# Optimization experiments

Hardware: AMD Instinct MI355X
Metric: run time of the kernel (lower is better)

Reference implementation:

```python
import jax, jax.numpy as jnp
import numpy as np

CODEBOOK_SIZE = 1024
CODEWORD_SIZE = 256
BETA = 0.1
N_INIT = 1  # embedding ~ U(-1/n, 1/n)


def setup_inputs() -> dict:
    key = jax.random.key(0)
    kx, ke = jax.random.split(key)
    x = jax.random.normal(kx, (16, 4096, CODEWORD_SIZE), dtype=jnp.float32)
    embedding = jax.random.uniform(
        ke, (CODEBOOK_SIZE, CODEWORD_SIZE), dtype=jnp.float32,
        minval=-1.0 / N_INIT, maxval=1.0 / N_INIT)
    return {"x": x, "embedding": embedding}


def reference(x, embedding):
    dist = (jnp.sum(x * x, axis=2, keepdims=True)
            + jnp.sum(embedding * embedding, axis=1)
            - 2.0 * jnp.einsum('btd,kd->btk', x, embedding))
    indexes = jnp.argmin(dist, axis=2)              # [B,T] int
    values = jnp.take(embedding, indexes, axis=0)   # gather == one_hot @ embedding
    sg = jax.lax.stop_gradient
    loss1 = jnp.mean((sg(x) - values) ** 2)         # codebook loss
    loss2 = jnp.mean((x - sg(values)) ** 2)         # commitment loss
    loss = loss1 + BETA * loss2
    values_st = x + sg(values - x)                  # straight-through
    return values_st, indexes, loss
```

## Files before the change

kernel.cpp:

```cpp
#include <hip/hip_runtime.h>
#include <stdint.h>


#define BT    65536
#define D     256
#define KCB   1024
#define BM    256
#define BN    256
#define NT    (KCB/BN)
#define BK    32
#define NSTEP (NT * (D / BK))

typedef float    f32x4 __attribute__((ext_vector_type(4)));
typedef _Float16 f16x8 __attribute__((ext_vector_type(8)));

#define GLOAD_LDS16(g, l) \
  __builtin_amdgcn_global_load_lds((const __attribute__((address_space(1))) void*)(g), \
                                   (__attribute__((address_space(3))) void*)(l), 16, 0, 0)

__global__ __launch_bounds__(256) void split_kernel(const float* __restrict__ src,
                                                    _Float16* __restrict__ dh,
                                                    _Float16* __restrict__ dl,
                                                    float* __restrict__ norm) {
    const int r = blockIdx.x * 8 + (threadIdx.x >> 5);
    const size_t i0 = (size_t)r * D + (threadIdx.x & 31) * 8;
    float4 v0 = *(const float4*)(src + i0);
    float4 v1 = *(const float4*)(src + i0 + 4);
    float v[8] = {v0.x, v0.y, v0.z, v0.w, v1.x, v1.y, v1.z, v1.w};
    f16x8 h, l;
    float s = 0.f;
    #pragma unroll
    for (int j = 0; j < 8; ++j) {
        _Float16 hh = (_Float16)v[j];
        h[j] = hh;
        l[j] = (_Float16)(v[j] - (float)hh);
        s += v[j] * v[j];
    }
    *(f16x8*)(dh + i0) = h;
    *(f16x8*)(dl + i0) = l;
    #pragma unroll
    for (int off = 1; off < 32; off <<= 1) s += __shfl_xor(s, off, 64);
    if ((threadIdx.x & 31) == 0) norm[r] = s;
}

__global__ __launch_bounds__(512, 2) void vq_mfma_kernel(
    const _Float16* __restrict__ Xh, const _Float16* __restrict__ Xl,
    const _Float16* __restrict__ Eh, const _Float16* __restrict__ El,
    const float* __restrict__ enorm, const float* __restrict__ xnorm,
    const float* __restrict__ E,
    float* __restrict__ out_vals, float* __restrict__ out_idx,
    float* __restrict__ out_loss) {
    __shared__ __align__(16) _Float16 Ash[2][BM * BK];
    __shared__ __align__(16) _Float16 Asl[2][BM * BK];
    __shared__ __align__(16) _Float16 Bsh[2][BN * BK];
    __shared__ __align__(16) _Float16 Bsl[2][BN * BK];
    __shared__ float s_en[KCB];
    __shared__ float s_bd[BM];
    __shared__ int   s_bi[BM];
    __shared__ float s_red[8];

    const int tid  = threadIdx.x;
    const int w    = tid >> 6;
    const int lane = tid & 63;
    const int quad = lane >> 4;
    const int l16  = lane & 15;
    const int wm   = w >> 1;
    const int wn   = w & 1;
    const int row0 = blockIdx.x * BM;

    const int sr = lane >> 2;
    const int sk = ((((lane & 3) - (lane >> 3)) & 3) << 3);
    const int kob = ((quad + ((l16 >> 1) & 3)) & 3) << 3;

    s_en[tid]       = enorm[tid];
    s_en[tid + 512] = enorm[tid + 512];

    auto STAGE = [&](int buf, int s) {
        const int kb   = (s & 7) * BK;
        const int col0 = (s >> 3) * BN;
        #pragma unroll
        for (int t = 0; t < 2; ++t) {
            const int chunk = w * 2 + t;
            const int gr = chunk * 16 + sr;
            const size_t ga = (size_t)(row0 + gr) * D + kb + sk;
            GLOAD_LDS16(Xh + ga, &Ash[buf][chunk * 512]);
            GLOAD_LDS16(Xl + ga, &Asl[buf][chunk * 512]);
            const size_t gb = (size_t)(col0 + gr) * D + kb + sk;
            GLOAD_LDS16(Eh + gb, &Bsh[buf][chunk * 512]);
            GLOAD_LDS16(El + gb, &Bsl[buf][chunk * 512]);
        }
    };

    float rb_d[4][4];
    int   rb_i[4][4];
    #pragma unroll
    for (int i = 0; i < 4; ++i)
        #pragma unroll
        for (int r = 0; r < 4; ++r) { rb_d[i][r] = 3.4e38f; rb_i[i][r] = 0; }
    f32x4 acc[4][8];

    STAGE(0, 0);
    asm volatile("s_waitcnt lgkmcnt(0)" ::: "memory");

    #pragma unroll 2
    for (int s = 0; s < NSTEP; ++s) {
        const int cur = s & 1;
        if (s + 1 < NSTEP) {
            STAGE(cur ^ 1, s + 1);
            asm volatile("s_waitcnt vmcnt(8)" ::: "memory");
        } else {
            asm volatile("s_waitcnt vmcnt(0)" ::: "memory");
        }
        __builtin_amdgcn_s_barrier();

        if ((s & 7) == 0) {
            #pragma unroll
            for (int i = 0; i < 4; ++i)
                #pragma unroll
                for (int j = 0; j < 8; ++j) acc[i][j] = (f32x4)0.0f;
        }

        const _Float16* Ah = Ash[cur];
        const _Float16* Al = Asl[cur];
        const _Float16* Bh = Bsh[cur];
        const _Float16* Bl = Bsl[cur];

        f16x8 ah[4], al[4];
        #pragma unroll
        for (int i = 0; i < 4; ++i) {
            const int ra = (wm * 64 + i * 16 + l16) * BK + kob;
            ah[i] = *(const f16x8*)&Ah[ra];
            al[i] = *(const f16x8*)&Al[ra];
        }

        __builtin_amdgcn_s_setprio(1);
        #pragma unroll
        for (int j = 0; j < 8; ++j) {
            const int n = (wn * 128 + j * 16 + l16) * BK + kob;
            const f16x8 bh = *(const f16x8*)&Bh[n];
            const f16x8 bl = *(const f16x8*)&Bl[n];
            #pragma unroll
            for (int i = 0; i < 4; ++i) {
                acc[i][j] = __builtin_amdgcn_mfma_f32_16x16x32_f16(ah[i], bh, acc[i][j], 0, 0, 0);
                acc[i][j] = __builtin_amdgcn_mfma_f32_16x16x32_f16(al[i], bh, acc[i][j], 0, 0, 0);
                acc[i][j] = __builtin_amdgcn_mfma_f32_16x16x32_f16(ah[i], bl, acc[i][j], 0, 0, 0);
            }
        }
        __builtin_amdgcn_s_setprio(0);

        if ((s & 7) == 7) {
            const int nt = s >> 3;
            #pragma unroll
            for (int j = 0; j < 8; ++j) {
                const int c = nt * BN + wn * 128 + j * 16 + l16;
                const float en = s_en[c];
                #pragma unroll
                for (int i = 0; i < 4; ++i)
                    #pragma unroll
                    for (int r = 0; r < 4; ++r) {
                        const float sd = en - 2.0f * acc[i][j][r];
                        if (sd < rb_d[i][r]) { rb_d[i][r] = sd; rb_i[i][r] = c; }
                    }
            }
        }
        __builtin_amdgcn_s_barrier();
    }

    #pragma unroll
    for (int off = 1; off < 16; off <<= 1) {
        #pragma unroll
        for (int i = 0; i < 4; ++i)
            #pragma unroll
            for (int r = 0; r < 4; ++r) {
                const float od = __shfl_xor(rb_d[i][r], off, 64);
                const int   oi = __shfl_xor(rb_i[i][r], off, 64);
                if (od < rb_d[i][r] || (od == rb_d[i][r] && oi < rb_i[i][r])) {
                    rb_d[i][r] = od; rb_i[i][r] = oi;
                }
            }
    }
    if (wn == 0 && l16 == 0) {
        #pragma unroll
        for (int i = 0; i < 4; ++i)
            #pragma unroll
            for (int r = 0; r < 4; ++r) {
                const int m = wm * 64 + i * 16 + quad * 4 + r;
                s_bd[m] = rb_d[i][r]; s_bi[m] = rb_i[i][r];
            }
    }
    __syncthreads();
    if (wn == 1 && l16 == 0) {
        #pragma unroll
        for (int i = 0; i < 4; ++i)
            #pragma unroll
            for (int r = 0; r < 4; ++r) {
                const int m = wm * 64 + i * 16 + quad * 4 + r;
                if (rb_d[i][r] < s_bd[m] || (rb_d[i][r] == s_bd[m] && rb_i[i][r] < s_bi[m])) {
                    s_bd[m] = rb_d[i][r]; s_bi[m] = rb_i[i][r];
                }
            }
    }
    __syncthreads();

    float part = 0.f;
    if (tid < BM) {
        out_idx[row0 + tid] = (float)s_bi[tid];
        part = xnorm[row0 + tid] + s_bd[tid];
    }

    const int col = tid & 255;
    const int sub = tid >> 8;
    #pragma unroll 4
    for (int it = 0; it < BM / 2; ++it) {
        const int r  = it * 2 + sub;
        const int bi = s_bi[r];
        out_vals[(size_t)(row0 + r) * D + col] = E[(size_t)bi * D + col];
    }

    #pragma unroll
    for (int off = 1; off < 64; off <<= 1) part += __shfl_xor(part, off, 64);
    if (lane == 0) s_red[w] = part;
    __syncthreads();
    if (tid == 0) {
        float tot = 0.f;
        #pragma unroll
        for (int i = 0; i < 8; ++i) tot += s_red[i];
        atomicAdd(out_loss, tot * (1.1f / 16777216.f));
    }
}

extern "C" void kernel_launch(void* const* d_in, const int* in_sizes, int n_in,
                              void* d_out, int out_size, void* d_ws, size_t ws_size,
                              hipStream_t stream) {
    const float* X = (const float*)d_in[0];
    const float* E = (const float*)d_in[1];
    float* out      = (float*)d_out;
    float* out_vals = out;
    float* out_idx  = out + (size_t)BT * D;
    float* out_loss = out + (size_t)BT * D + BT;

    char* ws = (char*)d_ws;
    _Float16* Eh    = (_Float16*)ws;
    _Float16* El    = Eh + (size_t)KCB * D;
    _Float16* Xh    = El + (size_t)KCB * D;
    _Float16* Xl    = Xh + (size_t)BT * D;
    float*    enorm = (float*)(Xl + (size_t)BT * D);
    float*    xnorm = enorm + KCB;
    (void)ws_size; (void)n_in; (void)in_sizes; (void)out_size;

    hipMemsetAsync(out_loss, 0, sizeof(float), stream);
    split_kernel<<<KCB / 8, 256, 0, stream>>>(E, Eh, El, enorm);
    split_kernel<<<BT / 8, 256, 0, stream>>>(X, Xh, Xl, xnorm);
    vq_mfma_kernel<<<BT / BM, 512, 0, stream>>>(Xh, Xl, Eh, El, enorm, xnorm, E,
                                                out_vals, out_idx, out_loss);
}
```

Baseline: 228.8 us.

## Fuse X fp16 split into GEMM kernel and pair MFMA groups with barriers

```diff
diff --git a/kernel.cpp b/kernel.cpp
--- a/kernel.cpp
+++ b/kernel.cpp
@@ -18,14 +18,16 @@
   __builtin_amdgcn_global_load_lds((const __attribute__((address_space(1))) void*)(g), \
                                    (__attribute__((address_space(3))) void*)(l), 16, 0, 0)
 
-__global__ __launch_bounds__(256) void split_kernel(const float* __restrict__ src,
-                                                    _Float16* __restrict__ dh,
-                                                    _Float16* __restrict__ dl,
-                                                    float* __restrict__ norm) {
+__global__ __launch_bounds__(256) void split_e_kernel(const float* __restrict__ E,
+                                                      _Float16* __restrict__ Eh,
+                                                      _Float16* __restrict__ El,
+                                                      float* __restrict__ enorm,
+                                                      float* __restrict__ out_loss) {
+    if (blockIdx.x == 0 && threadIdx.x == 0) *out_loss = 0.f;
     const int r = blockIdx.x * 8 + (threadIdx.x >> 5);
     const size_t i0 = (size_t)r * D + (threadIdx.x & 31) * 8;
-    float4 v0 = *(const float4*)(src + i0);
-    float4 v1 = *(const float4*)(src + i0 + 4);
+    float4 v0 = *(const float4*)(E + i0);
+    float4 v1 = *(const float4*)(E + i0 + 4);
     float v[8] = {v0.x, v0.y, v0.z, v0.w, v1.x, v1.y, v1.z, v1.w};
     f16x8 h, l;
     float s = 0.f;
@@ -36,22 +38,20 @@
         l[j] = (_Float16)(v[j] - (float)hh);
         s += v[j] * v[j];
     }
-    *(f16x8*)(dh + i0) = h;
-    *(f16x8*)(dl + i0) = l;
+    *(f16x8*)(Eh + i0) = h;
+    *(f16x8*)(El + i0) = l;
     #pragma unroll
     for (int off = 1; off < 32; off <<= 1) s += __shfl_xor(s, off, 64);
-    if ((threadIdx.x & 31) == 0) norm[r] = s;
+    if ((threadIdx.x & 31) == 0) enorm[r] = s;
 }
 
 __global__ __launch_bounds__(512, 2) void vq_mfma_kernel(
-    const _Float16* __restrict__ Xh, const _Float16* __restrict__ Xl,
+    const float* __restrict__ X,
     const _Float16* __restrict__ Eh, const _Float16* __restrict__ El,
-    const float* __restrict__ enorm, const float* __restrict__ xnorm,
-    const float* __restrict__ E,
+    const float* __restrict__ enorm, const float* __restrict__ E,
     float* __restrict__ out_vals, float* __restrict__ out_idx,
     float* __restrict__ out_loss) {
-    __shared__ __align__(16) _Float16 Ash[2][BM * BK];
-    __shared__ __align__(16) _Float16 Asl[2][BM * BK];
+    __shared__ __align__(16) float    Asf[2][BM * BK];
     __shared__ __align__(16) _Float16 Bsh[2][BN * BK];
     __shared__ __align__(16) _Float16 Bsl[2][BN * BK];
     __shared__ float s_en[KCB];
@@ -66,10 +66,13 @@
     const int l16  = lane & 15;
     const int wm   = w >> 1;
     const int wn   = w & 1;
+    const int sxa  = l16 & 7;
     const int row0 = blockIdx.x * BM;
 
-    const int sr = lane >> 2;
-    const int sk = ((((lane & 3) - (lane >> 3)) & 3) << 3);
+    const int sa_row = lane >> 3;
+    const int sa_off = ((lane & 7) ^ sa_row) * 4;
+    const int sb_row = lane >> 2;
+    const int sb_off = ((((lane & 3) - (lane >> 3)) & 3) << 3);
     const int kob = ((quad + ((l16 >> 1) & 3)) & 3) << 3;
 
     s_en[tid]       = enorm[tid];
@@ -79,13 +82,16 @@
         const int kb   = (s & 7) * BK;
         const int col0 = (s >> 3) * BN;
         #pragma unroll
+        for (int t = 0; t < 4; ++t) {
+            const int chunk = w * 4 + t;
+            const int gr = row0 + chunk * 8 + sa_row;
+            GLOAD_LDS16(X + (size_t)gr * D + kb + sa_off, &Asf[buf][chunk * 256]);
+        }
+        #pragma unroll
         for (int t = 0; t < 2; ++t) {
             const int chunk = w * 2 + t;
-            const int gr = chunk * 16 + sr;
-            const size_t ga = (size_t)(row0 + gr) * D + kb + sk;
-            GLOAD_LDS16(Xh + ga, &Ash[buf][chunk * 512]);
-            GLOAD_LDS16(Xl + ga, &Asl[buf][chunk * 512]);
-            const size_t gb = (size_t)(col0 + gr) * D + kb + sk;
+            const int gr = col0 + chunk * 16 + sb_row;
+            const size_t gb = (size_t)gr * D + kb + sb_off;
             GLOAD_LDS16(Eh + gb, &Bsh[buf][chunk * 512]);
             GLOAD_LDS16(El + gb, &Bsl[buf][chunk * 512]);
         }
@@ -97,6 +103,7 @@
     for (int i = 0; i < 4; ++i)
         #pragma unroll
         for (int r = 0; r < 4; ++r) { rb_d[i][r] = 3.4e38f; rb_i[i][r] = 0; }
+    float xs = 0.f;
     f32x4 acc[4][8];
 
     STAGE(0, 0);
@@ -120,33 +127,55 @@
                 for (int j = 0; j < 8; ++j) acc[i][j] = (f32x4)0.0f;
         }
 
-        const _Float16* Ah = Ash[cur];
-        const _Float16* Al = Asl[cur];
+        const float*    As = Asf[cur];
         const _Float16* Bh = Bsh[cur];
         const _Float16* Bl = Bsl[cur];
 
         f16x8 ah[4], al[4];
         #pragma unroll
         for (int i = 0; i < 4; ++i) {
-            const int ra = (wm * 64 + i * 16 + l16) * BK + kob;
-            ah[i] = *(const f16x8*)&Ah[ra];
-            al[i] = *(const f16x8*)&Al[ra];
-        }
-
-        __builtin_amdgcn_s_setprio(1);
-        #pragma unroll
-        for (int j = 0; j < 8; ++j) {
-            const int n = (wn * 128 + j * 16 + l16) * BK + kob;
-            const f16x8 bh = *(const f16x8*)&Bh[n];
-            const f16x8 bl = *(const f16x8*)&Bl[n];
+            const float* rp = As + (wm * 64 + i * 16 + l16) * BK;
+            const f32x4 v0 = *(const f32x4*)(rp + ((((quad << 1))     ^ sxa) << 2));
+            const f32x4 v1 = *(const f32x4*)(rp + ((((quad << 1) | 1) ^ sxa) << 2));
+            const float f[8] = {v0.x, v0.y, v0.z, v0.w, v1.x, v1.y, v1.z, v1.w};
+            #pragma unroll
+            for (int e = 0; e < 8; ++e) {
+                const _Float16 hh = (_Float16)f[e];
+                ah[i][e] = hh;
+                al[i][e] = (_Float16)(f[e] - (float)hh);
+            }
+            if (wn == 0 && s < 8) {
+                #pragma unroll
+                for (int e = 0; e < 8; ++e) xs += f[e] * f[e];
+            }
+        }
+
+        #pragma unroll
+        for (int jp = 0; jp < 4; ++jp) {
+            const int j0 = jp * 2, j1 = jp * 2 + 1;
+            const f16x8 bh0 = *(const f16x8*)&Bh[(wn * 128 + j0 * 16 + l16) * BK + kob];
+            const f16x8 bl0 = *(const f16x8*)&Bl[(wn * 128 + j0 * 16 + l16) * BK + kob];
+            const f16x8 bh1 = *(const f16x8*)&Bh[(wn * 128 + j1 * 16 + l16) * BK + kob];
+            const f16x8 bl1 = *(const f16x8*)&Bl[(wn * 128 + j1 * 16 + l16) * BK + kob];
+            __builtin_amdgcn_s_barrier();
+            asm volatile("s_waitcnt lgkmcnt(0)" ::: "memory");
+            __builtin_amdgcn_sched_barrier(0);
+            __builtin_amdgcn_s_setprio(1);
             #pragma unroll
             for (int i = 0; i < 4; ++i) {
-                acc[i][j] = __builtin_amdgcn_mfma_f32_16x16x32_f16(ah[i], bh, acc[i][j], 0, 0, 0);
-                acc[i][j] = __builtin_amdgcn_mfma_f32_16x16x32_f16(al[i], bh, acc[i][j], 0, 0, 0);
-                acc[i][j] = __builtin_amdgcn_mfma_f32_16x16x32_f16(ah[i], bl, acc[i][j], 0, 0, 0);
-            }
-        }
-        __builtin_amdgcn_s_setprio(0);
+                acc[i][j0] = __builtin_amdgcn_mfma_f32_16x16x32_f16(ah[i], bh0, acc[i][j0], 0, 0, 0);
+                acc[i][j0] = __builtin_amdgcn_mfma_f32_16x16x32_f16(al[i], bh0, acc[i][j0], 0, 0, 0);
+                acc[i][j0] = __builtin_amdgcn_mfma_f32_16x16x32_f16(ah[i], bl0, acc[i][j0], 0, 0, 0);
+            }
+            #pragma unroll
+            for (int i = 0; i < 4; ++i) {
+                acc[i][j1] = __builtin_amdgcn_mfma_f32_16x16x32_f16(ah[i], bh1, acc[i][j1], 0, 0, 0);
+                acc[i][j1] = __builtin_amdgcn_mfma_f32_16x16x32_f16(al[i], bh1, acc[i][j1], 0, 0, 0);
+                acc[i][j1] = __builtin_amdgcn_mfma_f32_16x16x32_f16(ah[i], bl1, acc[i][j1], 0, 0, 0);
+            }
+            __builtin_amdgcn_s_setprio(0);
+            __builtin_amdgcn_s_barrier();
+        }
 
         if ((s & 7) == 7) {
             const int nt = s >> 3;
@@ -163,7 +192,6 @@
                     }
             }
         }
-        __builtin_amdgcn_s_barrier();
     }
 
     #pragma unroll
@@ -202,10 +230,10 @@
     }
     __syncthreads();
 
-    float part = 0.f;
+    float part = xs;
     if (tid < BM) {
         out_idx[row0 + tid] = (float)s_bi[tid];
-        part = xnorm[row0 + tid] + s_bd[tid];
+        part += s_bd[tid];
     }
 
     const int col = tid & 255;
@@ -242,15 +270,10 @@
     char* ws = (char*)d_ws;
     _Float16* Eh    = (_Float16*)ws;
     _Float16* El    = Eh + (size_t)KCB * D;
-    _Float16* Xh    = El + (size_t)KCB * D;
-    _Float16* Xl    = Xh + (size_t)BT * D;
-    float*    enorm = (float*)(Xl + (size_t)BT * D);
-    float*    xnorm = enorm + KCB;
+    float*    enorm = (float*)(El + (size_t)KCB * D);
     (void)ws_size; (void)n_in; (void)in_sizes; (void)out_size;
 
-    hipMemsetAsync(out_loss, 0, sizeof(float), stream);
-    split_kernel<<<KCB / 8, 256, 0, stream>>>(E, Eh, El, enorm);
-    split_kernel<<<BT / 8, 256, 0, stream>>>(X, Xh, Xl, xnorm);
-    vq_mfma_kernel<<<BT / BM, 512, 0, stream>>>(Xh, Xl, Eh, El, enorm, xnorm, E,
+    split_e_kernel<<<KCB / 8, 256, 0, stream>>>(E, Eh, El, enorm, out_loss);
+    vq_mfma_kernel<<<BT / BM, 512, 0, stream>>>(X, Eh, El, enorm, E,
                                                 out_vals, out_idx, out_loss);
 }
```

Result: faster. 217.3 us (-5.0%).
